# Kernel tuning notes

Measured on AMD Instinct MI355X. Metric: run time of the kernel, lower is better.

The kernel has to match this reference:

```python
import jax, jax.numpy as jnp
import numpy as np

FEATURE_HEIGHT = 50
FEATURE_WIDTH = 50


def setup_inputs() -> dict:
    key = jax.random.key(0)
    k1, k2, k3 = jax.random.split(key, 3)
    bs, K, H, D = 16, FEATURE_HEIGHT * FEATURE_WIDTH, 8, 32
    Q, L, P = 2000, 1, 4
    value = jax.random.normal(k1, (bs, K, H, D), dtype=jnp.float32)
    value_spatial_shapes = jnp.array([[FEATURE_HEIGHT, FEATURE_WIDTH]], dtype=jnp.int64)
    sampling_locations = jax.random.uniform(k2, (bs, Q, H, L, P, 2), dtype=jnp.float32)
    attention_weights = jax.random.uniform(k3, (bs, Q, H, L, P), dtype=jnp.float32)
    return {
        "value": value,
        "value_spatial_shapes": value_spatial_shapes,
        "sampling_locations": sampling_locations,
        "attention_weights": attention_weights,
    }


def _bilinear_sample(img, grid):
    """torch.F.grid_sample(mode='bilinear', padding_mode='zeros', align_corners=False).

    img:  (N, D, h, w)
    grid: (N, Q, P, 2), last dim (x, y) in [-1, 1]
    returns (N, D, Q, P)
    """
    N, D, h, w = img.shape
    # unnormalize (align_corners=False)
    x = (grid[..., 0] + 1.0) * (w * 0.5) - 0.5  # (N, Q, P)
    y = (grid[..., 1] + 1.0) * (h * 0.5) - 0.5
    x0 = jnp.floor(x)
    y0 = jnp.floor(y)
    x1 = x0 + 1.0
    y1 = y0 + 1.0
    wx1 = x - x0
    wx0 = 1.0 - wx1
    wy1 = y - y0
    wy0 = 1.0 - wy1

    img_flat = img.reshape(N, D, h * w)

    def corner(ix, iy, wgt):
        valid = ((ix >= 0) & (ix < w) & (iy >= 0) & (iy < h)).astype(img.dtype)
        ixc = jnp.clip(ix, 0, w - 1).astype(jnp.int32)
        iyc = jnp.clip(iy, 0, h - 1).astype(jnp.int32)
        idx = (iyc * w + ixc).reshape(N, -1)  # (N, Q*P)
        vals = jnp.take_along_axis(img_flat, idx[:, None, :], axis=2)  # (N, D, Q*P)
        vals = vals.reshape(N, D, *ix.shape[1:])  # (N, D, Q, P)
        return vals * (wgt * valid)[:, None]

    out = corner(x0, y0, wx0 * wy0)
    out = out + corner(x1, y0, wx1 * wy0)
    out = out + corner(x0, y1, wx0 * wy1)
    out = out + corner(x1, y1, wx1 * wy1)
    return out


def reference(value, value_spatial_shapes, sampling_locations, attention_weights):
    bs, K, H, D = value.shape
    _, Q, _, L, P, _ = sampling_locations.shape
    h, w = FEATURE_HEIGHT, FEATURE_WIDTH

    sampling_grids = 2.0 * sampling_locations - 1.0  # (bs, Q, H, L, P, 2)
    # value -> (bs*H, D, h, w)
    v = value.reshape(bs, K, H * D).transpose(0, 2, 1).reshape(bs * H, D, h, w)
    # level 0 grid -> (bs*H, Q, P, 2)
    g = jnp.transpose(sampling_grids[:, :, :, 0], (0, 2, 1, 3, 4)).reshape(bs * H, Q, P, 2)
    sampled = _bilinear_sample(v, g)  # (bs*H, D, Q, P)
    # attention weights -> (bs*H, 1, Q, L*P)
    aw = jnp.transpose(attention_weights, (0, 2, 1, 3, 4)).reshape(bs * H, 1, Q, L * P)
    out = (sampled * aw).sum(-1)  # (bs*H, D, Q)
    out = out.reshape(bs, H * D, Q).transpose(0, 2, 1)  # (bs, Q, H*D)
    return out
```

## Files before the change

### kernel.cpp

```cpp
#include <hip/hip_runtime.h>


#define FH 50
#define FW 50
#define KK (FH * FW)
#define NH 8
#define ND 32
#define NQ 2000
#define NP 4

__global__ __launch_bounds__(256) void deform_attn_kernel(
    const float* __restrict__ value,
    const float* __restrict__ loc,
    const float* __restrict__ attw,
    float* __restrict__ out)
{
    const int g = blockIdx.x * 8 + (threadIdx.x >> 5);
    const int d = threadIdx.x & 31;
    const int h = g & (NH - 1);
    const int bq = g >> 3;
    const int b = bq / NQ;

    const float* __restrict__ vbase =
        value + ((size_t)b * KK * NH + (size_t)h) * ND + d;
    const float2* __restrict__ locp = (const float2*)(loc + (size_t)g * (NP * 2));
    const float* __restrict__ awp = attw + (size_t)g * NP;

    float acc = 0.f;
#pragma unroll
    for (int p = 0; p < NP; ++p) {
        const float2 l = locp[p];
        const float aw = awp[p];
        const float x = l.x * (float)FW - 0.5f;
        const float y = l.y * (float)FH - 0.5f;
        const float x0f = floorf(x);
        const float y0f = floorf(y);
        const int x0 = (int)x0f, y0 = (int)y0f;
        const int x1 = x0 + 1, y1 = y0 + 1;
        const float wx1 = x - x0f, wx0 = 1.f - wx1;
        const float wy1 = y - y0f, wy0 = 1.f - wy1;

        const bool vx0 = (x0 >= 0) && (x0 < FW);
        const bool vx1 = (x1 >= 0) && (x1 < FW);
        const bool vy0 = (y0 >= 0) && (y0 < FH);
        const bool vy1 = (y1 >= 0) && (y1 < FH);

        const int cx0 = min(max(x0, 0), FW - 1);
        const int cx1 = min(max(x1, 0), FW - 1);
        const int cy0 = min(max(y0, 0), FH - 1);
        const int cy1 = min(max(y1, 0), FH - 1);

        const float v00 = vbase[(size_t)(cy0 * FW + cx0) * (NH * ND)];
        const float v10 = vbase[(size_t)(cy0 * FW + cx1) * (NH * ND)];
        const float v01 = vbase[(size_t)(cy1 * FW + cx0) * (NH * ND)];
        const float v11 = vbase[(size_t)(cy1 * FW + cx1) * (NH * ND)];

        float s = 0.f;
        s += ((vx0 && vy0) ? (wx0 * wy0) : 0.f) * v00;
        s += ((vx1 && vy0) ? (wx1 * wy0) : 0.f) * v10;
        s += ((vx0 && vy1) ? (wx0 * wy1) : 0.f) * v01;
        s += ((vx1 && vy1) ? (wx1 * wy1) : 0.f) * v11;
        acc += aw * s;
    }

    out[(size_t)bq * (NH * ND) + h * ND + d] = acc;
}

extern "C" void kernel_launch(void* const* d_in, const int* in_sizes, int n_in,
                              void* d_out, int out_size, void* d_ws, size_t ws_size,
                              hipStream_t stream) {
    const float* value = (const float*)d_in[0];
    const float* loc  = (const float*)d_in[2];
    const float* attw = (const float*)d_in[3];
    float* out = (float*)d_out;

    const int bs = in_sizes[0] / (KK * NH * ND);
    const int groups = bs * NQ * NH;
    const int blocks = groups / 8;

    deform_attn_kernel<<<blocks, 256, 0, stream>>>(value, loc, attw, out);
}
```

Before: 128.9 us.

## Vectorize channel loads to float4 with 8 threads per head-query group

Each thread now handles four channels through float4 loads of value and a float4 store of the output, so a group of 8 threads covers the 32-dim head instead of 32 threads. Sampling locations and attention weights are read as float4 vectors, and the attention weight is folded into the bilinear corner weights. This cuts memory instructions and redundant per-thread coordinate math by 4x, at the cost of more registers per thread and fewer threads in total.

Measured after the change: 126.0 us. 2.2% less time.

```diff
diff --git a/kernel.cpp b/kernel.cpp
--- a/kernel.cpp
+++ b/kernel.cpp
@@ -15,24 +15,29 @@
     const float* __restrict__ attw,
     float* __restrict__ out)
 {
-    const int g = blockIdx.x * 8 + (threadIdx.x >> 5);
-    const int d = threadIdx.x & 31;
-    const int h = g & (NH - 1);
-    const int bq = g >> 3;
+    const int gid = blockIdx.x * 32 + (threadIdx.x >> 3);
+    const int c = threadIdx.x & 7;
+    const int h = gid & (NH - 1);
+    const int bq = gid >> 3;
     const int b = bq / NQ;
 
-    const float* __restrict__ vbase =
-        value + ((size_t)b * KK * NH + (size_t)h) * ND + d;
-    const float2* __restrict__ locp = (const float2*)(loc + (size_t)g * (NP * 2));
-    const float* __restrict__ awp = attw + (size_t)g * NP;
+    const float4* __restrict__ vbase =
+        (const float4*)value + ((size_t)b * KK * NH + (size_t)h) * (ND / 4) + c;
 
-    float acc = 0.f;
+    const float4* __restrict__ locp = (const float4*)loc + (size_t)gid * 2;
+    const float4 lv0 = locp[0];
+    const float4 lv1 = locp[1];
+    const float4 aw4 = ((const float4*)attw)[gid];
+
+    const float px[NP] = {lv0.x, lv0.z, lv1.x, lv1.z};
+    const float py[NP] = {lv0.y, lv0.w, lv1.y, lv1.w};
+    const float aw[NP] = {aw4.x, aw4.y, aw4.z, aw4.w};
+
+    float4 acc = {0.f, 0.f, 0.f, 0.f};
 #pragma unroll
     for (int p = 0; p < NP; ++p) {
-        const float2 l = locp[p];
-        const float aw = awp[p];
-        const float x = l.x * (float)FW - 0.5f;
-        const float y = l.y * (float)FH - 0.5f;
+        const float x = px[p] * (float)FW - 0.5f;
+        const float y = py[p] * (float)FH - 0.5f;
         const float x0f = floorf(x);
         const float y0f = floorf(y);
         const int x0 = (int)x0f, y0 = (int)y0f;
@@ -50,20 +55,23 @@
         const int cy0 = min(max(y0, 0), FH - 1);
         const int cy1 = min(max(y1, 0), FH - 1);
 
-        const float v00 = vbase[(size_t)(cy0 * FW + cx0) * (NH * ND)];
-        const float v10 = vbase[(size_t)(cy0 * FW + cx1) * (NH * ND)];
-        const float v01 = vbase[(size_t)(cy1 * FW + cx0) * (NH * ND)];
-        const float v11 = vbase[(size_t)(cy1 * FW + cx1) * (NH * ND)];
+        const float4 v00 = vbase[(size_t)(cy0 * FW + cx0) * (NH * ND / 4)];
+        const float4 v10 = vbase[(size_t)(cy0 * FW + cx1) * (NH * ND / 4)];
+        const float4 v01 = vbase[(size_t)(cy1 * FW + cx0) * (NH * ND / 4)];
+        const float4 v11 = vbase[(size_t)(cy1 * FW + cx1) * (NH * ND / 4)];
 
-        float s = 0.f;
-        s += ((vx0 && vy0) ? (wx0 * wy0) : 0.f) * v00;
-        s += ((vx1 && vy0) ? (wx1 * wy0) : 0.f) * v10;
-        s += ((vx0 && vy1) ? (wx0 * wy1) : 0.f) * v01;
-        s += ((vx1 && vy1) ? (wx1 * wy1) : 0.f) * v11;
-        acc += aw * s;
+        const float w00 = ((vx0 && vy0) ? (wx0 * wy0) : 0.f) * aw[p];
+        const float w10 = ((vx1 && vy0) ? (wx1 * wy0) : 0.f) * aw[p];
+        const float w01 = ((vx0 && vy1) ? (wx0 * wy1) : 0.f) * aw[p];
+        const float w11 = ((vx1 && vy1) ? (wx1 * wy1) : 0.f) * aw[p];
+
+        acc.x += w00 * v00.x + w10 * v10.x + w01 * v01.x + w11 * v11.x;
+        acc.y += w00 * v00.y + w10 * v10.y + w01 * v01.y + w11 * v11.y;
+        acc.z += w00 * v00.z + w10 * v10.z + w01 * v01.z + w11 * v11.z;
+        acc.w += w00 * v00.w + w10 * v10.w + w01 * v01.w + w11 * v11.w;
     }
 
-    out[(size_t)bq * (NH * ND) + h * ND + d] = acc;
+    ((float4*)out)[(size_t)bq * (NH * ND / 4) + h * (ND / 4) + c] = acc;
 }
 
 extern "C" void kernel_launch(void* const* d_in, const int* in_sizes, int n_in,
@@ -76,7 +84,7 @@
 
     const int bs = in_sizes[0] / (KK * NH * ND);
     const int groups = bs * NQ * NH;
-    const int blocks = groups / 8;
+    const int blocks = groups / 32;
 
     deform_attn_kernel<<<blocks, 256, 0, stream>>>(value, loc, attw, out);
 }
```
